# Optimization experiments

Hardware: AMD Instinct MI355X
Metric: run time of the kernel (lower is better)

Reference implementation:

```python
import jax, jax.numpy as jnp
import numpy as np


def setup_inputs() -> dict:
    key = jax.random.key(0)
    k1, k2, k3, k4, k5 = jax.random.split(key, 5)
    B, Ci, Co, H, W, N, K = 8, 256, 256, 128, 128, 4, 3
    x = jax.random.normal(k1, (B, Ci, H, W), dtype=jnp.float32)
    weight = jax.random.normal(k2, (N, Co, Ci, K, K), dtype=jnp.float32)
    styles = jax.random.normal(k3, (B, Ci), dtype=jnp.float32)
    selector = jax.random.uniform(k4, (B, N), dtype=jnp.float32)
    noise = jax.random.normal(k5, (B, Co, H, W), dtype=jnp.float32)
    return {"x": x, "weight": weight, "styles": styles,
            "selector": selector, "noise": noise}


def reference(x, weight, styles, selector, noise):
    """Modulated conv2d with adaptive kernel selection (fused_modconv path).

    x:        [B, Ci, H, W]
    weight:   [N, Co, Ci, kh, kw]  kernel bank
    styles:   [B, Ci]              modulation
    selector: [B, N]               adaptive kernel mixing coefficients
    noise:    [B, Co, H, W]        additive noise
    """
    B, Ci, H, W = x.shape
    N, Co, _, kh, kw = weight.shape

    # adaptive kernel selection: per-sample kernel = selector-weighted sum of bank
    w = jnp.einsum('bn,noihw->boihw', selector, weight)          # [B,Co,Ci,kh,kw]

    # modulate by styles
    w = w * styles[:, None, :, None, None]

    # demodulate
    dcoefs = jax.lax.rsqrt(jnp.sum(w * w, axis=(2, 3, 4)) + 1e-8)  # [B,Co]
    w = w * dcoefs[:, :, None, None, None]

    # fused per-sample conv via grouped conv (groups = B), cross-correlation
    # (flip_weight=True in the torch code means plain conv2d / cross-correlation)
    xr = x.reshape(1, B * Ci, H, W)
    wr = w.reshape(B * Co, Ci, kh, kw)
    out = jax.lax.conv_general_dilated(
        xr, wr,
        window_strides=(1, 1),
        padding=[(kh // 2, kh // 2), (kw // 2, kw // 2)],
        feature_group_count=B,
        dimension_numbers=('NCHW', 'OIHW', 'NCHW'),
    )
    out = out.reshape(B, Co, H, W) + noise
    return out
```

## Files before the change

### kernel.cpp

```cpp
#include <hip/hip_runtime.h>


typedef __attribute__((ext_vector_type(4))) float f32x4;
typedef __attribute__((ext_vector_type(8))) short s16x8;

#define NB   8
#define NCI  256
#define NCO  256
#define NHW  128
#define NKER 4

#define SB0 __builtin_amdgcn_sched_barrier(0)
#define BAR __builtin_amdgcn_s_barrier()
#define WAITV(N) asm volatile("s_waitcnt vmcnt(" #N ")" ::: "memory")
#define WAITL0   asm volatile("s_waitcnt lgkmcnt(0)" ::: "memory")

__device__ __forceinline__ unsigned short f2bf(float f) {
  unsigned int u = __builtin_bit_cast(unsigned int, f);
  u += 0x7FFFu + ((u >> 16) & 1u);
  return (unsigned short)(u >> 16);
}

__device__ __forceinline__ void gl_lds16(const void* g, void* l) {
  __builtin_amdgcn_global_load_lds(
      (const __attribute__((address_space(1))) void*)(unsigned long long)(uintptr_t)g,
      (__attribute__((address_space(3))) void*)(unsigned int)(uintptr_t)l,
      16, 0, 0);
}

__global__ __launch_bounds__(256) void prep_k(
    const float* __restrict__ weight,
    const float* __restrict__ styles,
    const float* __restrict__ selector,
    unsigned short* __restrict__ wmod)
{
  int bid = blockIdx.x;
  int b = bid >> 8, co = bid & 255;
  int ci = threadIdx.x;

  float sel[NKER];
#pragma unroll
  for (int n = 0; n < NKER; ++n) sel[n] = selector[b * NKER + n];

  float a[9];
#pragma unroll
  for (int j = 0; j < 9; ++j) a[j] = 0.f;
#pragma unroll
  for (int n = 0; n < NKER; ++n) {
    const float* wp = weight + (size_t)((n * NCO + co) * NCI + ci) * 9;
    float s = sel[n];
#pragma unroll
    for (int j = 0; j < 9; ++j) a[j] += s * wp[j];
  }
  float st = styles[b * NCI + ci];
  float ss = 0.f;
#pragma unroll
  for (int j = 0; j < 9; ++j) { a[j] *= st; ss += a[j] * a[j]; }

  for (int off = 32; off; off >>= 1) ss += __shfl_down(ss, off, 64);
  __shared__ float red[4];
  int wid = threadIdx.x >> 6, lane = threadIdx.x & 63;
  if (lane == 0) red[wid] = ss;
  __syncthreads();
  float tot = red[0] + red[1] + red[2] + red[3];
  float d = rsqrtf(tot + 1e-8f);

  int kb = ci >> 5, ci5 = ci & 31;
  int row = co >> 1;
  int slot = (((co & 1) << 2) + (ci5 >> 3)) ^ (row & 7);
  int boff = (slot << 4) + ((ci5 & 7) << 1);
#pragma unroll
  for (int j = 0; j < 9; ++j) {
    size_t T = (size_t)((b * 9 + j) * 8 + kb);
    wmod[(T << 13) + (row << 6) + (boff >> 1)] = f2bf(a[j] * d);
  }
}

__global__ __launch_bounds__(256, 2) void conv_k(
    const float* __restrict__ x,
    const unsigned short* __restrict__ wg,
    const float* __restrict__ noise,
    float* __restrict__ out)
{
  extern __shared__ __align__(16) char smem[];
  char* AlB = smem;
  char* XRs = smem + 3 * 16384;

  int orig = blockIdx.x;
  int b = orig & 7;
  int h = orig >> 3;

  int t = threadIdx.x;
  int lane = t & 63;
  int wid = t >> 6;
  int cow = wid << 6;
  int ll = lane & 15;
  int ks = lane >> 4;

  int dh0 = (h == 0) ? 1 : 0;
  int nseg = 3 - (h == 0) - (h == 127);
  int NG = nseg << 3;
  int NT = NG * 3;

  f32x4 acc[4][8];
#pragma unroll
  for (int m = 0; m < 4; ++m)
#pragma unroll
    for (int n = 0; n < 8; ++n) acc[m][n] = (f32x4){0.f, 0.f, 0.f, 0.f};

  int c = ((t >> 4) & 15) * 2;
  int wi = t & 15;
  float xlo[8], xhi[8];

  auto issueX = [&](int g) {
    int gc = g < NG ? g : NG - 1;
    int dh = dh0 + (gc >> 3);
    int kb = gc & 7;
    int hy = h + dh - 1;
    const float* base = x + ((size_t)(b * NCI + kb * 32 + c) * NHW + hy) * NHW + wi;
#pragma unroll
    for (int j2 = 0; j2 < 8; ++j2) {
      xlo[j2] = base[j2 * 16];
      xhi[j2] = base[NHW * NHW + j2 * 16];
    }
  };

  auto issueA = [&](int tauc, int buf) {
    int gg = tauc / 3;
    int tap = tauc - gg * 3;
    int dh = dh0 + (gg >> 3);
    int kb = gg & 7;
    const char* src = (const char*)wg +
        ((size_t)((b * 9 + dh * 3 + tap) * 8 + kb) << 14);
    char* dst = AlB + buf * 16384;
#pragma unroll
    for (int i = 0; i < 4; ++i) {
      int ch = wid * 4 + i;
      gl_lds16(src + ch * 1024 + lane * 16, dst + ch * 1024 + lane * 16);
    }
  };

  auto packXR = [&](int g) {
    char* dstb = XRs + (g & 1) * 8192;
    int slot = (((wi & 1) << 2) + (c >> 3)) ^ ((wi >> 1) & 7);
    char* p0 = dstb + (wi >> 1) * 128 + (slot << 4) + ((c & 7) << 1);
#pragma unroll
    for (int j2 = 0; j2 < 8; ++j2) {
      unsigned int pk = ((unsigned)f2bf(xhi[j2]) << 16) | f2bf(xlo[j2]);
      *(unsigned int*)(p0 + j2 * 1024) = pk;
    }
  };

  auto readA = [&](int buf, s16x8* af) {
    const char* Ab = AlB + buf * 16384;
#pragma unroll
    for (int m = 0; m < 4; ++m) {
      int co = cow + m * 16 + ll;
      int row = co >> 1;
      int slot = (((co & 1) << 2) + ks) ^ (row & 7);
      af[m] = *(const s16x8*)(Ab + row * 128 + (slot << 4));
    }
  };
  auto readB = [&](int xrb, int dw, s16x8* bf) {
    const char* Xb = XRs + xrb * 8192;
#pragma unroll
    for (int n = 0; n < 8; ++n) {
      int wn = n * 16 + ll + dw - 1;
      if ((dw == 0 && n == 0) || (dw == 2 && n == 7)) {
        int wx = wn < 0 ? 0 : (wn > 127 ? 127 : wn);
        int row = wx >> 1;
        int slot = (((wx & 1) << 2) + ks) ^ (row & 7);
        s16x8 bv = *(const s16x8*)(Xb + row * 128 + (slot << 4));
        if (wn != wx) { s16x8 z = {0, 0, 0, 0, 0, 0, 0, 0}; bv = z; }
        bf[n] = bv;
      } else {
        int row = wn >> 1;
        int slot = (((wn & 1) << 2) + ks) ^ (row & 7);
        bf[n] = *(const s16x8*)(Xb + row * 128 + (slot << 4));
      }
    }
  };
  auto mfma32 = [&](s16x8* af, s16x8* bf) {
    __builtin_amdgcn_s_setprio(1);
#pragma unroll
    for (int m = 0; m < 4; ++m)
#pragma unroll
      for (int n = 0; n < 8; ++n)
        acc[m][n] = __builtin_amdgcn_mfma_f32_16x16x32_bf16(
            af[m], bf[n], acc[m][n], 0, 0, 0);
    __builtin_amdgcn_s_setprio(0);
  };

  issueX(0); SB0;
  issueA(0, 0); SB0;
  issueA(1, 1); SB0;
  WAITV(8); SB0;
  packXR(0);
  WAITV(4); SB0;
  WAITL0; SB0;
  BAR; SB0;

#pragma unroll 1
  for (int g = 0; g < NG; ++g) {
    int xrb = g & 1;
    int tau = g * 3;
    {
      s16x8 af[4], bf[8];
      readA(0, af); readB(xrb, 0, bf);
      issueA(tau + 2, 2); SB0;
      issueX(g + 1); SB0;
      BAR; WAITL0; SB0;
      mfma32(af, bf);
      WAITV(20); SB0;
      BAR; SB0;
    }
    {
      s16x8 af[4], bf[8];
      readA(1, af); readB(xrb, 1, bf);
      int tc = tau + 3; if (tc > NT - 1) tc = NT - 1;
      issueA(tc, 0); SB0;
      BAR; WAITL0; SB0;
      mfma32(af, bf);
      WAITV(20); SB0;
      BAR; SB0;
    }
    {
      s16x8 af[4], bf[8];
      readA(2, af); readB(xrb, 2, bf);
      int tc = tau + 4; if (tc > NT - 1) tc = NT - 1;
      issueA(tc, 1); SB0;
      WAITV(4); SB0;
      packXR(g + 1);
      BAR; WAITL0; SB0;
      mfma32(af, bf);
      BAR; SB0;
    }
  }

  int pr4 = ks * 4;
#pragma unroll
  for (int m = 0; m < 4; ++m) {
#pragma unroll
    for (int n = 0; n < 8; ++n) {
      int px = n * 16 + ll;
#pragma unroll
      for (int j = 0; j < 4; ++j) {
        int co = cow + m * 16 + pr4 + j;
        size_t idx = ((size_t)(b * NCO + co) * NHW + h) * NHW + px;
        out[idx] = acc[m][n][j] + noise[idx];
      }
    }
  }
}

extern "C" void kernel_launch(void* const* d_in, const int* in_sizes, int n_in,
                              void* d_out, int out_size, void* d_ws, size_t ws_size,
                              hipStream_t stream) {
  const float* x        = (const float*)d_in[0];
  const float* weight   = (const float*)d_in[1];
  const float* styles   = (const float*)d_in[2];
  const float* selector = (const float*)d_in[3];
  const float* noise    = (const float*)d_in[4];
  float* out = (float*)d_out;

  unsigned short* wmod = (unsigned short*)d_ws;

  hipLaunchKernelGGL(prep_k, dim3(NB * NCO), dim3(256), 0, stream,
                     weight, styles, selector, wmod);
  hipLaunchKernelGGL(conv_k, dim3(NB * NHW), dim3(256), 64 * 1024, stream,
                     x, wmod, noise, out);
}
```

Before: 189.1 us.

## Software-pipeline B-fragment LDS reads across taps and unify boundary rows

New measurement: 204.8 us. +8.3%, slower.

```diff
diff --git a/kernel.cpp b/kernel.cpp
--- a/kernel.cpp
+++ b/kernel.cpp
@@ -97,11 +97,6 @@
   int ll = lane & 15;
   int ks = lane >> 4;
 
-  int dh0 = (h == 0) ? 1 : 0;
-  int nseg = 3 - (h == 0) - (h == 127);
-  int NG = nseg << 3;
-  int NT = NG * 3;
-
   f32x4 acc[4][8];
 #pragma unroll
   for (int m = 0; m < 4; ++m)
@@ -111,13 +106,15 @@
   int c = ((t >> 4) & 15) * 2;
   int wi = t & 15;
   float xlo[8], xhi[8];
+  unsigned xmask = 0xFFFFFFFFu;
 
   auto issueX = [&](int g) {
-    int gc = g < NG ? g : NG - 1;
-    int dh = dh0 + (gc >> 3);
-    int kb = gc & 7;
+    int gc = g < 24 ? g : 23;
+    int dh = gc >> 3, kb = gc & 7;
     int hy = h + dh - 1;
-    const float* base = x + ((size_t)(b * NCI + kb * 32 + c) * NHW + hy) * NHW + wi;
+    xmask = ((unsigned)hy < 128u) ? 0xFFFFFFFFu : 0u;
+    int hyc = hy < 0 ? 0 : (hy > 127 ? 127 : hy);
+    const float* base = x + ((size_t)(b * NCI + kb * 32 + c) * NHW + hyc) * NHW + wi;
 #pragma unroll
     for (int j2 = 0; j2 < 8; ++j2) {
       xlo[j2] = base[j2 * 16];
@@ -125,14 +122,12 @@
     }
   };
 
-  auto issueA = [&](int tauc, int buf) {
-    int gg = tauc / 3;
-    int tap = tauc - gg * 3;
-    int dh = dh0 + (gg >> 3);
-    int kb = gg & 7;
+  auto issueA = [&](int tc, char* dst) {
+    if (tc > 71) tc = 71;
+    int g = tc / 3, tap = tc - g * 3;
+    int dh = g >> 3, kb = g & 7;
     const char* src = (const char*)wg +
         ((size_t)((b * 9 + dh * 3 + tap) * 8 + kb) << 14);
-    char* dst = AlB + buf * 16384;
 #pragma unroll
     for (int i = 0; i < 4; ++i) {
       int ch = wid * 4 + i;
@@ -146,13 +141,12 @@
     char* p0 = dstb + (wi >> 1) * 128 + (slot << 4) + ((c & 7) << 1);
 #pragma unroll
     for (int j2 = 0; j2 < 8; ++j2) {
-      unsigned int pk = ((unsigned)f2bf(xhi[j2]) << 16) | f2bf(xlo[j2]);
-      *(unsigned int*)(p0 + j2 * 1024) = pk;
-    }
-  };
-
-  auto readA = [&](int buf, s16x8* af) {
-    const char* Ab = AlB + buf * 16384;
+      unsigned pk = ((unsigned)f2bf(xhi[j2]) << 16) | f2bf(xlo[j2]);
+      *(unsigned*)(p0 + j2 * 1024) = pk & xmask;
+    }
+  };
+
+  auto readAF = [&](const char* Ab, s16x8* af) {
 #pragma unroll
     for (int m = 0; m < 4; ++m) {
       int co = cow + m * 16 + ll;
@@ -161,80 +155,92 @@
       af[m] = *(const s16x8*)(Ab + row * 128 + (slot << 4));
     }
   };
-  auto readB = [&](int xrb, int dw, s16x8* bf) {
-    const char* Xb = XRs + xrb * 8192;
-#pragma unroll
-    for (int n = 0; n < 8; ++n) {
-      int wn = n * 16 + ll + dw - 1;
-      if ((dw == 0 && n == 0) || (dw == 2 && n == 7)) {
-        int wx = wn < 0 ? 0 : (wn > 127 ? 127 : wn);
-        int row = wx >> 1;
-        int slot = (((wx & 1) << 2) + ks) ^ (row & 7);
-        s16x8 bv = *(const s16x8*)(Xb + row * 128 + (slot << 4));
-        if (wn != wx) { s16x8 z = {0, 0, 0, 0, 0, 0, 0, 0}; bv = z; }
-        bf[n] = bv;
-      } else {
-        int row = wn >> 1;
-        int slot = (((wn & 1) << 2) + ks) ^ (row & 7);
-        bf[n] = *(const s16x8*)(Xb + row * 128 + (slot << 4));
-      }
-    }
-  };
-  auto mfma32 = [&](s16x8* af, s16x8* bf) {
-    __builtin_amdgcn_s_setprio(1);
-#pragma unroll
-    for (int m = 0; m < 4; ++m)
-#pragma unroll
-      for (int n = 0; n < 8; ++n)
-        acc[m][n] = __builtin_amdgcn_mfma_f32_16x16x32_bf16(
-            af[m], bf[n], acc[m][n], 0, 0, 0);
-    __builtin_amdgcn_s_setprio(0);
-  };
+
+#define PFB(XRBASE, DW, bf)                                              \
+  {                                                                      \
+    const char* Xb = (XRBASE);                                           \
+    _Pragma("unroll")                                                    \
+    for (int n = 0; n < 8; ++n) {                                        \
+      int wn = n * 16 + ll + (DW) - 1;                                   \
+      if (((DW) == 0 && n == 0) || ((DW) == 2 && n == 7)) {              \
+        int wx = wn < 0 ? 0 : (wn > 127 ? 127 : wn);                     \
+        int row = wx >> 1;                                               \
+        int slot = (((wx & 1) << 2) + ks) ^ (row & 7);                   \
+        s16x8 bv = *(const s16x8*)(Xb + row * 128 + (slot << 4));        \
+        if (wn != wx) { s16x8 z = {0, 0, 0, 0, 0, 0, 0, 0}; bv = z; }    \
+        bf[n] = bv;                                                      \
+      } else {                                                           \
+        int row = wn >> 1;                                               \
+        int slot = (((wn & 1) << 2) + ks) ^ (row & 7);                   \
+        bf[n] = *(const s16x8*)(Xb + row * 128 + (slot << 4));           \
+      }                                                                  \
+    }                                                                    \
+  }
+
+#define MFMA32(af, bf)                                                   \
+  __builtin_amdgcn_s_setprio(1);                                         \
+  _Pragma("unroll")                                                      \
+  for (int m = 0; m < 4; ++m)                                            \
+    _Pragma("unroll")                                                    \
+    for (int n = 0; n < 8; ++n)                                          \
+      acc[m][n] = __builtin_amdgcn_mfma_f32_16x16x32_bf16(               \
+          af[m], bf[n], acc[m][n], 0, 0, 0);                             \
+  __builtin_amdgcn_s_setprio(0);
+
+  s16x8 bfA[8], bfB[8], af[4];
 
   issueX(0); SB0;
-  issueA(0, 0); SB0;
-  issueA(1, 1); SB0;
+  issueA(0, AlB); SB0;
+  issueA(1, AlB + 16384); SB0;
   WAITV(8); SB0;
   packXR(0);
   WAITV(4); SB0;
   WAITL0; SB0;
   BAR; SB0;
+  PFB(XRs, 0, bfA);
 
 #pragma unroll 1
-  for (int g = 0; g < NG; ++g) {
-    int xrb = g & 1;
-    int tau = g * 3;
-    {
-      s16x8 af[4], bf[8];
-      readA(0, af); readB(xrb, 0, bf);
-      issueA(tau + 2, 2); SB0;
-      issueX(g + 1); SB0;
-      BAR; WAITL0; SB0;
-      mfma32(af, bf);
-      WAITV(20); SB0;
-      BAR; SB0;
-    }
-    {
-      s16x8 af[4], bf[8];
-      readA(1, af); readB(xrb, 1, bf);
-      int tc = tau + 3; if (tc > NT - 1) tc = NT - 1;
-      issueA(tc, 0); SB0;
-      BAR; WAITL0; SB0;
-      mfma32(af, bf);
-      WAITV(20); SB0;
-      BAR; SB0;
-    }
-    {
-      s16x8 af[4], bf[8];
-      readA(2, af); readB(xrb, 2, bf);
-      int tc = tau + 4; if (tc > NT - 1) tc = NT - 1;
-      issueA(tc, 1); SB0;
-      WAITV(4); SB0;
-      packXR(g + 1);
-      BAR; WAITL0; SB0;
-      mfma32(af, bf);
-      BAR; SB0;
-    }
+  for (int gg = 0; gg < 12; ++gg) {
+    int t0 = gg * 6;
+    int g0 = gg * 2;
+    WAITV(4); SB0; BAR; SB0;
+    issueA(t0 + 2, AlB + 2 * 16384); SB0;
+    issueX(g0 + 1); SB0;
+    readAF(AlB, af);
+    PFB(XRs, 1, bfB);
+    MFMA32(af, bfA);
+    WAITV(20); SB0; BAR; SB0;
+    issueA(t0 + 3, AlB); SB0;
+    WAITV(4); SB0;
+    packXR(g0 + 1);
+    readAF(AlB + 16384, af);
+    PFB(XRs, 2, bfA);
+    MFMA32(af, bfB);
+    WAITL0; SB0;
+    WAITV(4); SB0; BAR; SB0;
+    issueA(t0 + 4, AlB + 16384); SB0;
+    readAF(AlB + 2 * 16384, af);
+    PFB(XRs + 8192, 0, bfB);
+    MFMA32(af, bfA);
+    WAITV(4); SB0; BAR; SB0;
+    issueA(t0 + 5, AlB + 2 * 16384); SB0;
+    issueX(g0 + 2); SB0;
+    readAF(AlB, af);
+    PFB(XRs + 8192, 1, bfA);
+    MFMA32(af, bfB);
+    WAITV(20); SB0; BAR; SB0;
+    issueA(t0 + 6, AlB); SB0;
+    WAITV(4); SB0;
+    packXR(g0 + 2);
+    readAF(AlB + 16384, af);
+    PFB(XRs + 8192, 2, bfB);
+    MFMA32(af, bfA);
+    WAITL0; SB0;
+    WAITV(4); SB0; BAR; SB0;
+    issueA(t0 + 7, AlB + 16384); SB0;
+    readAF(AlB + 2 * 16384, af);
+    PFB(XRs, 0, bfA);
+    MFMA32(af, bfB);
   }
 
   int pr4 = ks * 4;
```
